# Performance work log

Measured on AMD Instinct MI355X. Metric: run time of the kernel, lower is better.

## Reference

```python
import jax, jax.numpy as jnp
import numpy as np

B, S, D = 8, 2048, 256


def setup_inputs() -> dict:
    key = jax.random.key(0)
    k1, k2, k3, k4, k5 = jax.random.split(key, 5)
    head = jax.random.normal(k1, (B, S, D), dtype=jnp.float32)
    dep = jax.random.normal(k2, (B, S, D), dtype=jnp.float32)
    edge_U = jax.random.normal(k3, (D, D), dtype=jnp.float32) / np.sqrt(D)
    edge_W = jax.random.normal(k4, (1, 2 * D), dtype=jnp.float32) / np.sqrt(2 * D)
    edge_b = jax.random.normal(k5, (1,), dtype=jnp.float32)
    return {"head": head, "dep": dep, "edge_U": edge_U, "edge_W": edge_W, "edge_b": edge_b}


def reference(head, dep, edge_U, edge_W, edge_b):
    # t1[b,i,o] = head[b,i,:] @ U @ dep[b,o,:]  -> [B,S,S]
    t1 = jnp.einsum('bid,de,boe->bio', head, edge_U, dep)
    # t2: linear over pairwise concat(head_i, dep_o); decomposes into two
    # broadcast-added matvecs (same math as W @ concat, no [B,S^2,2D] tensor).
    d = head.shape[-1]
    wh, wd = edge_W[0, :d], edge_W[0, d:]
    hs = head @ wh  # [B,S]
    ds = dep @ wd   # [B,S]
    t2 = hs[:, :, None] + ds[:, None, :]  # [B,S,S]
    return t1 + t2 + edge_b[0]
```

## Files before the change

### kernel.cpp

```cpp
#include <hip/hip_runtime.h>
#include <hip/hip_bf16.h>
#include <stdint.h>
#include <stddef.h>

#define B_ 8
#define S_ 2048
#define D_ 256

typedef __attribute__((ext_vector_type(8))) short short8;
typedef __attribute__((ext_vector_type(4))) float f32x4;

__device__ __forceinline__ short bf16of(float f) {
  union { float f; unsigned u; } x; x.f = f;
  unsigned r = x.u + 0x7FFFu + ((x.u >> 16) & 1u);
  return (short)(r >> 16);
}

__device__ __forceinline__ void async_ld16(const void* g, void* s) {
  __builtin_amdgcn_global_load_lds(
      (const __attribute__((address_space(1))) void*)g,
      (__attribute__((address_space(3))) void*)s, 16, 0, 0);
}

__global__ void k_prep_u(const float* __restrict__ U, short* __restrict__ UT) {
  int n = blockIdx.x;
  int k = threadIdx.x;
  UT[n * D_ + k] = bf16of(U[k * D_ + n]);
}

__launch_bounds__(256, 2)
__global__ void k_ahat(const float* __restrict__ head,
                       const short* __restrict__ UT,
                       const float* __restrict__ W,
                       short* __restrict__ Ahat,
                       float* __restrict__ hs) {
  __shared__ __align__(16) short sA[128 * 32];
  __shared__ __align__(16) short sB[128 * 32];
  const int t = threadIdx.x;
  const int w = t >> 6;
  const int l = t & 63;
  const int ntile = blockIdx.x;
  const int mbase = blockIdx.y * 128;
  const int nbase = ntile * 128;

  f32x4 acc[4][4];
#pragma unroll
  for (int i = 0; i < 4; ++i)
#pragma unroll
    for (int j = 0; j < 4; ++j) acc[i][j] = (f32x4)0.0f;

  float hsacc0 = 0.f, hsacc1 = 0.f;
  const int row0 = t >> 2;
  const int cc   = t & 3;

  for (int kb = 0; kb < 8; ++kb) {
    const int kbase = kb * 32;
    __syncthreads();
#pragma unroll
    for (int c = 0; c < 2; ++c) {
      int q = c * 256 + t;
      int r = q >> 2, qc = q & 3;
      async_ld16(UT + (nbase + r) * D_ + kbase + qc * 8, (char*)sB + q * 16);
    }
#pragma unroll
    for (int c = 0; c < 2; ++c) {
      int r = 64 * c + row0;
      const float4* gp = (const float4*)(head + (size_t)(mbase + r) * D_ + kbase + cc * 8);
      float4 v0 = gp[0], v1 = gp[1];
      const float4* wp = (const float4*)(W + kbase + cc * 8);
      float4 w0 = wp[0], w1 = wp[1];
      float p = v0.x * w0.x + v0.y * w0.y + v0.z * w0.z + v0.w * w0.w
              + v1.x * w1.x + v1.y * w1.y + v1.z * w1.z + v1.w * w1.w;
      if (c == 0) hsacc0 += p; else hsacc1 += p;
      short8 pk;
      pk[0] = bf16of(v0.x); pk[1] = bf16of(v0.y); pk[2] = bf16of(v0.z); pk[3] = bf16of(v0.w);
      pk[4] = bf16of(v1.x); pk[5] = bf16of(v1.y); pk[6] = bf16of(v1.z); pk[7] = bf16of(v1.w);
      *(short8*)(&sA[(64 * c + row0) * 32 + cc * 8]) = pk;
    }
    __syncthreads();

    const short8* pA = (const short8*)sA;
    const short8* pB = (const short8*)sB;
    const int arow = ((w >> 1) * 64) + (l & 15);
    const int brow = ((w & 1) * 64) + (l & 15);
    const int quad = l >> 4;
    short8 aF[4], bF[4];
#pragma unroll
    for (int mt = 0; mt < 4; ++mt) aF[mt] = pA[(arow + mt * 16) * 4 + quad];
#pragma unroll
    for (int nt = 0; nt < 4; ++nt) bF[nt] = pB[(brow + nt * 16) * 4 + quad];
#pragma unroll
    for (int mt = 0; mt < 4; ++mt)
#pragma unroll
      for (int nt = 0; nt < 4; ++nt)
        acc[mt][nt] = __builtin_amdgcn_mfma_f32_16x16x32_bf16(aF[mt], bF[nt], acc[mt][nt], 0, 0, 0);
  }

  {
    float v = hsacc0;
    v += __shfl_xor(v, 1);
    v += __shfl_xor(v, 2);
    if (cc == 0 && ntile == 0) hs[mbase + row0] = v;
    float u = hsacc1;
    u += __shfl_xor(u, 1);
    u += __shfl_xor(u, 2);
    if (cc == 0 && ntile == 0) hs[mbase + 64 + row0] = u;
  }

  const int quad = l >> 4;
#pragma unroll
  for (int mt = 0; mt < 4; ++mt) {
#pragma unroll
    for (int r = 0; r < 4; ++r) {
      int grow = mbase + (w >> 1) * 64 + mt * 16 + quad * 4 + r;
#pragma unroll
      for (int nt = 0; nt < 4; ++nt) {
        int gcol = nbase + (w & 1) * 64 + nt * 16 + (l & 15);
        Ahat[(size_t)grow * D_ + gcol] = bf16of(acc[mt][nt][r]);
      }
    }
  }
}

__launch_bounds__(256, 2)
__global__ void k_main(const short* __restrict__ Ahat,
                       const float* __restrict__ dep,
                       const float* __restrict__ W,
                       const float* __restrict__ hs,
                       const float* __restrict__ eb,
                       float* __restrict__ out) {
  __shared__ __align__(16) short sA[128 * 32];
  __shared__ __align__(16) short sB[128 * 32];
  __shared__ float hs_s[128];
  __shared__ float ds_s[128];
  const int t = threadIdx.x;
  const int w = t >> 6;
  const int l = t & 63;
  const int b = blockIdx.z;
  const int mbase = blockIdx.y * 128;
  const int nbase = blockIdx.x * 128;
  const float* wd = W + D_;

  if (t < 128) hs_s[t] = hs[b * S_ + mbase + t];

  f32x4 acc[4][4];
#pragma unroll
  for (int i = 0; i < 4; ++i)
#pragma unroll
    for (int j = 0; j < 4; ++j) acc[i][j] = (f32x4)0.0f;

  float dsacc0 = 0.f, dsacc1 = 0.f;
  const int row0 = t >> 2;
  const int cc   = t & 3;

  for (int kb = 0; kb < 8; ++kb) {
    const int kbase = kb * 32;
    __syncthreads();
#pragma unroll
    for (int c = 0; c < 2; ++c) {
      int q = c * 256 + t;
      int r = q >> 2, qc = q & 3;
      async_ld16(Ahat + (size_t)(b * S_ + mbase + r) * D_ + kbase + qc * 8, (char*)sA + q * 16);
    }
#pragma unroll
    for (int c = 0; c < 2; ++c) {
      int r = 64 * c + row0;
      const float4* gp = (const float4*)(dep + (size_t)(b * S_ + nbase + r) * D_ + kbase + cc * 8);
      float4 v0 = gp[0], v1 = gp[1];
      const float4* wp = (const float4*)(wd + kbase + cc * 8);
      float4 w0 = wp[0], w1 = wp[1];
      float p = v0.x * w0.x + v0.y * w0.y + v0.z * w0.z + v0.w * w0.w
              + v1.x * w1.x + v1.y * w1.y + v1.z * w1.z + v1.w * w1.w;
      if (c == 0) dsacc0 += p; else dsacc1 += p;
      short8 pk;
      pk[0] = bf16of(v0.x); pk[1] = bf16of(v0.y); pk[2] = bf16of(v0.z); pk[3] = bf16of(v0.w);
      pk[4] = bf16of(v1.x); pk[5] = bf16of(v1.y); pk[6] = bf16of(v1.z); pk[7] = bf16of(v1.w);
      *(short8*)(&sB[(64 * c + row0) * 32 + cc * 8]) = pk;
    }
    __syncthreads();

    const short8* pA = (const short8*)sA;
    const short8* pB = (const short8*)sB;
    const int arow = ((w >> 1) * 64) + (l & 15);
    const int brow = ((w & 1) * 64) + (l & 15);
    const int quad = l >> 4;
    short8 aF[4], bF[4];
#pragma unroll
    for (int mt = 0; mt < 4; ++mt) aF[mt] = pA[(arow + mt * 16) * 4 + quad];
#pragma unroll
    for (int nt = 0; nt < 4; ++nt) bF[nt] = pB[(brow + nt * 16) * 4 + quad];
#pragma unroll
    for (int mt = 0; mt < 4; ++mt)
#pragma unroll
      for (int nt = 0; nt < 4; ++nt)
        acc[mt][nt] = __builtin_amdgcn_mfma_f32_16x16x32_bf16(aF[mt], bF[nt], acc[mt][nt], 0, 0, 0);
  }

  {
    float v = dsacc0;
    v += __shfl_xor(v, 1);
    v += __shfl_xor(v, 2);
    if (cc == 0) ds_s[row0] = v;
    float u = dsacc1;
    u += __shfl_xor(u, 1);
    u += __shfl_xor(u, 2);
    if (cc == 0) ds_s[64 + row0] = u;
  }
  __syncthreads();

  const float bias = eb[0];
  const int quad = l >> 4;
#pragma unroll
  for (int mt = 0; mt < 4; ++mt) {
#pragma unroll
    for (int r = 0; r < 4; ++r) {
      int lrow = (w >> 1) * 64 + mt * 16 + quad * 4 + r;
      float hv = hs_s[lrow] + bias;
      int grow = b * S_ + mbase + lrow;
      float* orow = out + (size_t)grow * S_ + nbase;
#pragma unroll
      for (int nt = 0; nt < 4; ++nt) {
        int lcol = (w & 1) * 64 + nt * 16 + (l & 15);
        orow[lcol] = acc[mt][nt][r] + hv + ds_s[lcol];
      }
    }
  }
}

extern "C" void kernel_launch(void* const* d_in, const int* in_sizes, int n_in,
                              void* d_out, int out_size, void* d_ws, size_t ws_size,
                              hipStream_t stream) {
  const float* head = (const float*)d_in[0];
  const float* dep  = (const float*)d_in[1];
  const float* U    = (const float*)d_in[2];
  const float* W    = (const float*)d_in[3];
  const float* eb   = (const float*)d_in[4];
  float* out = (float*)d_out;

  char* ws = (char*)d_ws;
  short* UT   = (short*)ws;
  float* hs   = (float*)(ws + (128 << 10));
  short* Ahat = (short*)(ws + (192 << 10));

  k_prep_u<<<dim3(256), dim3(256), 0, stream>>>(U, UT);
  k_ahat<<<dim3(2, 128), dim3(256), 0, stream>>>(head, UT, W, Ahat, hs);
  k_main<<<dim3(16, 16, 8), dim3(256), 0, stream>>>(Ahat, dep, W, hs, eb, out);
}
```

Baseline: 212.4 us.

## Precompute bf16 inputs and row dot products in a separate pass

A new k_rows kernel converts head and dep to bf16 once and computes the hs/ds matvecs. This removes the repeated fp32 loads and conversions from the GEMM kernels, which load dep 16 times per batch in k_main. Both GEMMs now stage data with async global-to-LDS loads over larger K chunks, and operands are swapped so that output stores become float4-vectorized. The cost is an extra launch and extra workspace traffic for the bf16 copies, larger LDS use, and a raised occupancy hint of 3 blocks per SM on k_main.

```diff
diff --git a/kernel.cpp b/kernel.cpp
--- a/kernel.cpp
+++ b/kernel.cpp
@@ -6,8 +6,10 @@
 #define B_ 8
 #define S_ 2048
 #define D_ 256
+#define NROWS (B_ * S_)
 
 typedef __attribute__((ext_vector_type(8))) short short8;
+typedef __attribute__((ext_vector_type(4))) short short4v;
 typedef __attribute__((ext_vector_type(4))) float f32x4;
 
 __device__ __forceinline__ short bf16of(float f) {
@@ -28,20 +30,37 @@
   UT[n * D_ + k] = bf16of(U[k * D_ + n]);
 }
 
+__global__ void k_rows(const float* __restrict__ head, const float* __restrict__ dep,
+                       const float* __restrict__ W,
+                       float* __restrict__ hs, float* __restrict__ ds,
+                       short* __restrict__ headB, short* __restrict__ depB) {
+  const float* X; const float* wv; float* sv; short* XB;
+  if (blockIdx.y == 0) { X = head; wv = W;      sv = hs; XB = headB; }
+  else                 { X = dep;  wv = W + D_; sv = ds; XB = depB;  }
+  const int row = blockIdx.x * 4 + (threadIdx.x >> 6);
+  const int l = threadIdx.x & 63;
+  const float4 v  = *(const float4*)(X + (size_t)row * D_ + l * 4);
+  const float4 wq = *(const float4*)(wv + l * 4);
+  short4v pk;
+  pk[0] = bf16of(v.x); pk[1] = bf16of(v.y); pk[2] = bf16of(v.z); pk[3] = bf16of(v.w);
+  *(short4v*)(XB + (size_t)row * D_ + l * 4) = pk;
+  float p = v.x * wq.x + v.y * wq.y + v.z * wq.z + v.w * wq.w;
+  p += __shfl_xor(p, 1); p += __shfl_xor(p, 2); p += __shfl_xor(p, 4);
+  p += __shfl_xor(p, 8); p += __shfl_xor(p, 16); p += __shfl_xor(p, 32);
+  if (l == 0) sv[row] = p;
+}
+
 __launch_bounds__(256, 2)
-__global__ void k_ahat(const float* __restrict__ head,
-                       const short* __restrict__ UT,
-                       const float* __restrict__ W,
-                       short* __restrict__ Ahat,
-                       float* __restrict__ hs) {
-  __shared__ __align__(16) short sA[128 * 32];
-  __shared__ __align__(16) short sB[128 * 32];
+__global__ void k_ahat(const short* __restrict__ headB, const short* __restrict__ UT,
+                       short* __restrict__ Ahat) {
+  __shared__ __align__(16) short sU[4 * 128 * 32];
+  __shared__ __align__(16) short sH[4 * 128 * 32];
   const int t = threadIdx.x;
   const int w = t >> 6;
   const int l = t & 63;
-  const int ntile = blockIdx.x;
+  const int quad = l >> 4;
+  const int nbase = blockIdx.x * 128;
   const int mbase = blockIdx.y * 128;
-  const int nbase = ntile * 128;
 
   f32x4 acc[4][4];
 #pragma unroll
@@ -49,99 +68,71 @@
 #pragma unroll
     for (int j = 0; j < 4; ++j) acc[i][j] = (f32x4)0.0f;
 
-  float hsacc0 = 0.f, hsacc1 = 0.f;
-  const int row0 = t >> 2;
-  const int cc   = t & 3;
-
-  for (int kb = 0; kb < 8; ++kb) {
-    const int kbase = kb * 32;
-    __syncthreads();
-#pragma unroll
-    for (int c = 0; c < 2; ++c) {
-      int q = c * 256 + t;
-      int r = q >> 2, qc = q & 3;
-      async_ld16(UT + (nbase + r) * D_ + kbase + qc * 8, (char*)sB + q * 16);
-    }
-#pragma unroll
-    for (int c = 0; c < 2; ++c) {
-      int r = 64 * c + row0;
-      const float4* gp = (const float4*)(head + (size_t)(mbase + r) * D_ + kbase + cc * 8);
-      float4 v0 = gp[0], v1 = gp[1];
-      const float4* wp = (const float4*)(W + kbase + cc * 8);
-      float4 w0 = wp[0], w1 = wp[1];
-      float p = v0.x * w0.x + v0.y * w0.y + v0.z * w0.z + v0.w * w0.w
-              + v1.x * w1.x + v1.y * w1.y + v1.z * w1.z + v1.w * w1.w;
-      if (c == 0) hsacc0 += p; else hsacc1 += p;
-      short8 pk;
-      pk[0] = bf16of(v0.x); pk[1] = bf16of(v0.y); pk[2] = bf16of(v0.z); pk[3] = bf16of(v0.w);
-      pk[4] = bf16of(v1.x); pk[5] = bf16of(v1.y); pk[6] = bf16of(v1.z); pk[7] = bf16of(v1.w);
-      *(short8*)(&sA[(64 * c + row0) * 32 + cc * 8]) = pk;
-    }
-    __syncthreads();
-
-    const short8* pA = (const short8*)sA;
-    const short8* pB = (const short8*)sB;
-    const int arow = ((w >> 1) * 64) + (l & 15);
-    const int brow = ((w & 1) * 64) + (l & 15);
-    const int quad = l >> 4;
-    short8 aF[4], bF[4];
-#pragma unroll
-    for (int mt = 0; mt < 4; ++mt) aF[mt] = pA[(arow + mt * 16) * 4 + quad];
-#pragma unroll
-    for (int nt = 0; nt < 4; ++nt) bF[nt] = pB[(brow + nt * 16) * 4 + quad];
-#pragma unroll
-    for (int mt = 0; mt < 4; ++mt)
+  for (int it = 0; it < 2; ++it) {
+    __syncthreads();
+#pragma unroll
+    for (int kb = 0; kb < 4; ++kb) {
+#pragma unroll
+      for (int c = 0; c < 2; ++c) {
+        int q = c * 256 + t;
+        int r = q >> 2, qc = q & 3;
+        int kk = it * 128 + kb * 32 + qc * 8;
+        async_ld16(UT + (size_t)(nbase + r) * D_ + kk, (char*)sU + kb * 8192 + q * 16);
+        async_ld16(headB + (size_t)(mbase + r) * D_ + kk, (char*)sH + kb * 8192 + q * 16);
+      }
+    }
+    __syncthreads();
+    const short8* pU = (const short8*)sU;
+    const short8* pH = (const short8*)sH;
+#pragma unroll
+    for (int kb = 0; kb < 4; ++kb) {
+      short8 aF[4], bF[4];
+#pragma unroll
+      for (int mt = 0; mt < 4; ++mt)
+        aF[mt] = pU[(kb * 128 + (w >> 1) * 64 + mt * 16 + (l & 15)) * 4 + quad];
 #pragma unroll
       for (int nt = 0; nt < 4; ++nt)
-        acc[mt][nt] = __builtin_amdgcn_mfma_f32_16x16x32_bf16(aF[mt], bF[nt], acc[mt][nt], 0, 0, 0);
-  }
-
-  {
-    float v = hsacc0;
-    v += __shfl_xor(v, 1);
-    v += __shfl_xor(v, 2);
-    if (cc == 0 && ntile == 0) hs[mbase + row0] = v;
-    float u = hsacc1;
-    u += __shfl_xor(u, 1);
-    u += __shfl_xor(u, 2);
-    if (cc == 0 && ntile == 0) hs[mbase + 64 + row0] = u;
-  }
-
-  const int quad = l >> 4;
+        bF[nt] = pH[(kb * 128 + (w & 1) * 64 + nt * 16 + (l & 15)) * 4 + quad];
+#pragma unroll
+      for (int mt = 0; mt < 4; ++mt)
+#pragma unroll
+        for (int nt = 0; nt < 4; ++nt)
+          acc[mt][nt] = __builtin_amdgcn_mfma_f32_16x16x32_bf16(aF[mt], bF[nt], acc[mt][nt], 0, 0, 0);
+    }
+  }
+
 #pragma unroll
   for (int mt = 0; mt < 4; ++mt) {
-#pragma unroll
-    for (int r = 0; r < 4; ++r) {
-      int grow = mbase + (w >> 1) * 64 + mt * 16 + quad * 4 + r;
-#pragma unroll
-      for (int nt = 0; nt < 4; ++nt) {
-        int gcol = nbase + (w & 1) * 64 + nt * 16 + (l & 15);
-        Ahat[(size_t)grow * D_ + gcol] = bf16of(acc[mt][nt][r]);
-      }
-    }
-  }
-}
-
-__launch_bounds__(256, 2)
-__global__ void k_main(const short* __restrict__ Ahat,
-                       const float* __restrict__ dep,
-                       const float* __restrict__ W,
-                       const float* __restrict__ hs,
-                       const float* __restrict__ eb,
-                       float* __restrict__ out) {
-  __shared__ __align__(16) short sA[128 * 32];
-  __shared__ __align__(16) short sB[128 * 32];
+    int n_loc = (w >> 1) * 64 + mt * 16 + quad * 4;
+#pragma unroll
+    for (int nt = 0; nt < 4; ++nt) {
+      int i_loc = (w & 1) * 64 + nt * 16 + (l & 15);
+      short4v pk;
+      pk[0] = bf16of(acc[mt][nt][0]); pk[1] = bf16of(acc[mt][nt][1]);
+      pk[2] = bf16of(acc[mt][nt][2]); pk[3] = bf16of(acc[mt][nt][3]);
+      *(short4v*)(Ahat + (size_t)(mbase + i_loc) * D_ + nbase + n_loc) = pk;
+    }
+  }
+}
+
+__launch_bounds__(256, 3)
+__global__ void k_main(const short* __restrict__ Ahat, const short* __restrict__ depB,
+                       const float* __restrict__ hs, const float* __restrict__ ds,
+                       const float* __restrict__ eb, float* __restrict__ out) {
+  __shared__ __align__(16) short sA[2 * 128 * 32];
+  __shared__ __align__(16) short sD[2 * 128 * 32];
   __shared__ float hs_s[128];
   __shared__ float ds_s[128];
   const int t = threadIdx.x;
   const int w = t >> 6;
   const int l = t & 63;
+  const int quad = l >> 4;
   const int b = blockIdx.z;
   const int mbase = blockIdx.y * 128;
   const int nbase = blockIdx.x * 128;
-  const float* wd = W + D_;
 
   if (t < 128) hs_s[t] = hs[b * S_ + mbase + t];
+  else         ds_s[t - 128] = ds[b * S_ + nbase + t - 128];
 
   f32x4 acc[4][4];
 #pragma unroll
@@ -149,80 +140,55 @@
 #pragma unroll
     for (int j = 0; j < 4; ++j) acc[i][j] = (f32x4)0.0f;
 
-  float dsacc0 = 0.f, dsacc1 = 0.f;
-  const int row0 = t >> 2;
-  const int cc   = t & 3;
-
-  for (int kb = 0; kb < 8; ++kb) {
-    const int kbase = kb * 32;
-    __syncthreads();
-#pragma unroll
-    for (int c = 0; c < 2; ++c) {
-      int q = c * 256 + t;
-      int r = q >> 2, qc = q & 3;
-      async_ld16(Ahat + (size_t)(b * S_ + mbase + r) * D_ + kbase + qc * 8, (char*)sA + q * 16);
-    }
-#pragma unroll
-    for (int c = 0; c < 2; ++c) {
-      int r = 64 * c + row0;
-      const float4* gp = (const float4*)(dep + (size_t)(b * S_ + nbase + r) * D_ + kbase + cc * 8);
-      float4 v0 = gp[0], v1 = gp[1];
-      const float4* wp = (const float4*)(wd + kbase + cc * 8);
-      float4 w0 = wp[0], w1 = wp[1];
-      float p = v0.x * w0.x + v0.y * w0.y + v0.z * w0.z + v0.w * w0.w
-              + v1.x * w1.x + v1.y * w1.y + v1.z * w1.z + v1.w * w1.w;
-      if (c == 0) dsacc0 += p; else dsacc1 += p;
-      short8 pk;
-      pk[0] = bf16of(v0.x); pk[1] = bf16of(v0.y); pk[2] = bf16of(v0.z); pk[3] = bf16of(v0.w);
-      pk[4] = bf16of(v1.x); pk[5] = bf16of(v1.y); pk[6] = bf16of(v1.z); pk[7] = bf16of(v1.w);
-      *(short8*)(&sB[(64 * c + row0) * 32 + cc * 8]) = pk;
-    }
-    __syncthreads();
-
+  for (int it = 0; it < 4; ++it) {
+    __syncthreads();
+#pragma unroll
+    for (int kb = 0; kb < 2; ++kb) {
+#pragma unroll
+      for (int c = 0; c < 2; ++c) {
+        int q = c * 256 + t;
+        int r = q >> 2, qc = q & 3;
+        int kk = it * 64 + kb * 32 + qc * 8;
+        async_ld16(Ahat + (size_t)(b * S_ + mbase + r) * D_ + kk, (char*)sA + kb * 8192 + q * 16);
+        async_ld16(depB + (size_t)(b * S_ + nbase + r) * D_ + kk, (char*)sD + kb * 8192 + q * 16);
+      }
+    }
+    __syncthreads();
     const short8* pA = (const short8*)sA;
-    const short8* pB = (const short8*)sB;
-    const int arow = ((w >> 1) * 64) + (l & 15);
-    const int brow = ((w & 1) * 64) + (l & 15);
-    const int quad = l >> 4;
-    short8 aF[4], bF[4];
-#pragma unroll
-    for (int mt = 0; mt < 4; ++mt) aF[mt] = pA[(arow + mt * 16) * 4 + quad];
-#pragma unroll
-    for (int nt = 0; nt < 4; ++nt) bF[nt] = pB[(brow + nt * 16) * 4 + quad];
-#pragma unroll
-    for (int mt = 0; mt < 4; ++mt)
+    const short8* pD = (const short8*)sD;
+#pragma unroll
+    for (int kb = 0; kb < 2; ++kb) {
+      short8 aF[4], bF[4];
+#pragma unroll
+      for (int mt = 0; mt < 4; ++mt)
+        aF[mt] = pD[(kb * 128 + (w >> 1) * 64 + mt * 16 + (l & 15)) * 4 + quad];
 #pragma unroll
       for (int nt = 0; nt < 4; ++nt)
-        acc[mt][nt] = __builtin_amdgcn_mfma_f32_16x16x32_bf16(aF[mt], bF[nt], acc[mt][nt], 0, 0, 0);
-  }
-
-  {
-    float v = dsacc0;
-    v += __shfl_xor(v, 1);
-    v += __shfl_xor(v, 2);
-    if (cc == 0) ds_s[row0] = v;
-    float u = dsacc1;
-    u += __shfl_xor(u, 1);
-    u += __shfl_xor(u, 2);
-    if (cc == 0) ds_s[64 + row0] = u;
-  }
-  __syncthreads();
+        bF[nt] = pA[(kb * 128 + (w & 1) * 64 + nt * 16 + (l & 15)) * 4 + quad];
+#pragma unroll
+      for (int mt = 0; mt < 4; ++mt)
+#pragma unroll
+        for (int nt = 0; nt < 4; ++nt)
+          acc[mt][nt] = __builtin_amdgcn_mfma_f32_16x16x32_bf16(aF[mt], bF[nt], acc[mt][nt], 0, 0, 0);
+    }
+  }
 
   const float bias = eb[0];
-  const int quad = l >> 4;
 #pragma unroll
   for (int mt = 0; mt < 4; ++mt) {
-#pragma unroll
-    for (int r = 0; r < 4; ++r) {
-      int lrow = (w >> 1) * 64 + mt * 16 + quad * 4 + r;
-      float hv = hs_s[lrow] + bias;
-      int grow = b * S_ + mbase + lrow;
-      float* orow = out + (size_t)grow * S_ + nbase;
-#pragma unroll
-      for (int nt = 0; nt < 4; ++nt) {
-        int lcol = (w & 1) * 64 + nt * 16 + (l & 15);
-        orow[lcol] = acc[mt][nt][r] + hv + ds_s[lcol];
-      }
+    int o_loc = (w >> 1) * 64 + mt * 16 + quad * 4;
+    float4 dsv = *(const float4*)&ds_s[o_loc];
+#pragma unroll
+    for (int nt = 0; nt < 4; ++nt) {
+      int i_loc = (w & 1) * 64 + nt * 16 + (l & 15);
+      float hv = hs_s[i_loc] + bias;
+      f32x4 a = acc[mt][nt];
+      float4 o4;
+      o4.x = a[0] + hv + dsv.x;
+      o4.y = a[1] + hv + dsv.y;
+      o4.z = a[2] + hv + dsv.z;
+      o4.w = a[3] + hv + dsv.w;
+      *(float4*)(out + (size_t)(b * S_ + mbase + i_loc) * S_ + nbase + o_loc) = o4;
     }
   }
 }
@@ -238,11 +204,15 @@
   float* out = (float*)d_out;
 
   char* ws = (char*)d_ws;
-  short* UT   = (short*)ws;
-  float* hs   = (float*)(ws + (128 << 10));
-  short* Ahat = (short*)(ws + (192 << 10));
+  short* UT    = (short*)ws;
+  float* hs    = (float*)(ws + (128 << 10));
+  float* ds    = (float*)(ws + (192 << 10));
+  short* headB = (short*)(ws + (256 << 10));
+  short* depB  = (short*)(ws + (256 << 10) + (8 << 20));
+  short* Ahat  = (short*)(ws + (256 << 10) + (16 << 20));
 
   k_prep_u<<<dim3(256), dim3(256), 0, stream>>>(U, UT);
-  k_ahat<<<dim3(2, 128), dim3(256), 0, stream>>>(head, UT, W, Ahat, hs);
-  k_main<<<dim3(16, 16, 8), dim3(256), 0, stream>>>(Ahat, dep, W, hs, eb, out);
-}
+  k_rows<<<dim3(NROWS / 4, 2), dim3(256), 0, stream>>>(head, dep, W, hs, ds, headB, depB);
+  k_ahat<<<dim3(2, 128), dim3(256), 0, stream>>>(headB, UT, Ahat);
+  k_main<<<dim3(16, 16, 8), dim3(256), 0, stream>>>(Ahat, depB, hs, ds, eb, out);
+}
```

Measured after the change: 191.2 us. 10.0% less time.
